# Kernel optimization log

Measured on AMD Instinct MI355X. Metric: run time of the kernel, lower is better.

## Reference

```python
import jax, jax.numpy as jnp
import numpy as np

EPS = 1e-20
TEMP = 0.07
PATCH = 64
STEP = 32  # patch_size * overlap(0.5)


def zero_softmax(x, eps=1e-5):
    # ZeroSoftmax: ((exp(x)-1)^2) / (sum + eps), maps x==0 -> exactly 0 weight
    e = jnp.square(jnp.exp(x) - 1.0)
    return e / (jnp.sum(e, axis=-1, keepdims=True) + eps)


def _scaling_mask(H, W, p, step):
    # constant overlap-count mask from CRW.compute_scaling_mask (static shapes)
    sm = np.zeros((H, W), np.float32)
    for i in range(0, H - step, step):
        for j in range(0, W - step, step):
            sm[i:i + p, j:j + p] += 1.0
    return jnp.asarray(sm)


def _window_sums(m, p, step):
    # m: (B,T,SP,H,W) -> sliding-window sums (B,T,SP,nH,nW) via integral image
    ii = jnp.cumsum(jnp.cumsum(m, axis=-2), axis=-1)
    ii = jnp.pad(ii, ((0, 0), (0, 0), (0, 0), (1, 0), (1, 0)))
    H = m.shape[-2]
    nH = (H - p) // step + 1
    lo = jnp.arange(nH) * step
    hi = lo + p
    r_hi = ii[..., hi, :]   # (B,T,SP,nH,W+1)
    r_lo = ii[..., lo, :]
    return r_hi[..., hi] - r_hi[..., lo] - r_lo[..., hi] + r_lo[..., lo]


def setup_inputs() -> dict:
    key = jax.random.key(0)
    k1, k2, k3 = jax.random.split(key, 3)
    B, T, H, W = 2, 4, 256, 256
    nH = (H - PATCH) // STEP + 1  # 7
    N = nH * nH                   # 49 patches
    Cenc, D, SP = 512, 128, 64
    feats = jax.random.normal(k1, (B, N, Cenc, T), jnp.float32)
    W_head = jax.random.normal(k2, (Cenc, D), jnp.float32) / np.sqrt(Cenc)
    sp_mask = jax.random.randint(k3, (B, T, H, W), 0, SP, jnp.int32)
    return {"feats": feats, "W_head": W_head, "sp_mask": sp_mask, "max_sp_num": SP}


def reference(feats, W_head, sp_mask, max_sp_num):
    B, N, Cenc, T = feats.shape
    H, W = sp_mask.shape[-2:]
    SP = max_sp_num

    # --- pixels_to_nodes tail: projection head + L2 normalize over channel dim ---
    q = jnp.einsum('bnct,cd->bndt', feats, W_head)            # (B,N,128,T)
    nrm = jnp.maximum(jnp.linalg.norm(q, axis=2, keepdims=True), 1e-12)
    q = q / nrm
    q = jnp.transpose(q, (0, 2, 3, 1))                        # (B,128,T,N)

    # --- patches_to_sp_embeddings: windowed superpixel pooling ---
    oh = (sp_mask[:, :, None, :, :] ==
          jnp.arange(SP, dtype=sp_mask.dtype)[None, None, :, None, None]
          ).astype(jnp.float32)                               # (B,T,SP,H,W)
    sm = _scaling_mask(H, W, PATCH, STEP)                     # (H,W)
    ws = _window_sums(oh / sm, PATCH, STEP)                   # (B,T,SP,nH,nW)
    denom = jnp.sum(oh, axis=(-1, -2)) + EPS                  # (B,T,SP)
    wts = jnp.transpose(ws, (0, 1, 3, 4, 2)) / denom[:, :, None, None, :]
    wts = wts.reshape(B, T, N, SP)                            # (B,T,N,SP)
    q_sp = jnp.einsum('bdtn,btns->bdts', q, wts)              # (B,128,T,SP)

    # --- affinity + zero_softmax stochastic matrices ---
    As = jnp.einsum('bdtn,bdtm->btnm', q_sp[:, :, :-1], q_sp[:, :, 1:])  # (B,T-1,SP,SP)
    A12 = zero_softmax(As / TEMP)
    A21 = zero_softmax(jnp.swapaxes(As, -1, -2) / TEMP)

    # --- palindrome random walks + cross-entropy to cycle-consistency targets ---
    tgt = jnp.tile(jnp.arange(SP), B)
    loss = jnp.float32(0.0)
    AAs = []
    for i in range(1, T - 1):
        mats = [A12[:, k] for k in range(i + 1)] + [A21[:, k] for k in range(i, -1, -1)]
        aa = mats[0]
        for m in mats[1:]:
            aa = aa @ m
        AAs.append(aa)
        logits = jnp.log(aa + EPS).reshape(B * SP, SP)
        logp = jax.nn.log_softmax(logits, axis=-1)
        loss = loss + jnp.mean(-logp[jnp.arange(B * SP), tgt])
    return loss, jnp.stack(AAs)
```

## Files before the change

kernel.cpp:

```cpp
#include <hip/hip_runtime.h>
#include <hip/hip_bf16.h>

constexpr int NWIN = 49;
constexpr int QLD  = 52;

constexpr int OFF_WS   = 0;
constexpr int OFF_Q    = 26624;
constexpr int OFF_QSP  = 79872;
constexpr int OFF_A12  = 145408;
constexpr int OFF_A12T = 169984;
constexpr int OFF_A21  = 194560;
constexpr int OFF_A21T = 219136;
constexpr int OFF_R1T  = 251904;
constexpr int OFF_L    = 260096;
constexpr int OFF_BAR  = 276480;

__global__ void __launch_bounds__(256, 1)
k_front(const int* __restrict__ mask, const float* __restrict__ feats,
        const float* __restrict__ Wh, float* __restrict__ ws, float* __restrict__ q) {
    if (blockIdx.x < 392) {
        int win = blockIdx.x % NWIN;
        int bt  = blockIdx.x / NWIN;
        int wy = win / 7, wx = win % 7;
        __shared__ float loc[64];
        if (threadIdx.x < 64) loc[threadIdx.x] = 0.f;
        __syncthreads();
        const int* base = mask + bt * 65536 + (wy * 32) * 256 + wx * 32;
        #pragma unroll
        for (int it = 0; it < 16; ++it) {
            int idx = it * 256 + (int)threadIdx.x;
            int r = idx >> 6, c = idx & 63;
            int s = base[r * 256 + c];
            int y = wy * 32 + r, x = wx * 32 + c;
            float w = 1.f;
            if (y >= 32 && y < 224) w *= 0.5f;
            if (x >= 32 && x < 224) w *= 0.5f;
            atomicAdd(&loc[s], w);
        }
        __syncthreads();
        if (threadIdx.x < 64) {
            ws[(bt * 64 + (int)threadIdx.x) * QLD + win] = loc[threadIdx.x];
        } else if (win == 0) {
            int s = threadIdx.x & 63;
            int col = 49 + (int)(threadIdx.x >> 6) - 1;
            ws[(bt * 64 + s) * QLD + col] = 0.f;
        }
    } else {
        int bid = blockIdx.x - 392;
        int n = bid % NWIN, b = bid / NWIN;
        __shared__ float4 f4[512];
        __shared__ float4 psum4[512];
        __shared__ float4 red4[2];
        const float4* fp4 = (const float4*)(feats + (size_t)(b * NWIN + n) * 2048);
        for (int i = threadIdx.x; i < 512; i += 256) f4[i] = fp4[i];
        __syncthreads();

        int dl = threadIdx.x & 63, ch = threadIdx.x >> 6;
        float a0 = 0.f, a1 = 0.f, a2 = 0.f, a3 = 0.f;
        float b0 = 0.f, b1 = 0.f, b2 = 0.f, b3 = 0.f;
        const float* wpa = Wh + dl;
        const float* wpb = Wh + dl + 64;
        int c0 = ch * 128;
        #pragma unroll 8
        for (int c = c0; c < c0 + 128; ++c) {
            float w0 = wpa[c * 128];
            float w1 = wpb[c * 128];
            float4 fv = f4[c];
            a0 += fv.x * w0; a1 += fv.y * w0; a2 += fv.z * w0; a3 += fv.w * w0;
            b0 += fv.x * w1; b1 += fv.y * w1; b2 += fv.z * w1; b3 += fv.w * w1;
        }
        psum4[ch * 128 + dl]      = make_float4(a0, a1, a2, a3);
        psum4[ch * 128 + dl + 64] = make_float4(b0, b1, b2, b3);
        __syncthreads();

        float4 A;
        if (threadIdx.x < 128) {
            float4 p0 = psum4[threadIdx.x],       p1 = psum4[128 + threadIdx.x];
            float4 p2 = psum4[256 + threadIdx.x], p3 = psum4[384 + threadIdx.x];
            A = make_float4((p0.x + p1.x) + (p2.x + p3.x),
                            (p0.y + p1.y) + (p2.y + p3.y),
                            (p0.z + p1.z) + (p2.z + p3.z),
                            (p0.w + p1.w) + (p2.w + p3.w));
            float sx = A.x * A.x, sy = A.y * A.y, sz = A.z * A.z, sw = A.w * A.w;
            for (int off = 32; off; off >>= 1) {
                sx += __shfl_down(sx, off); sy += __shfl_down(sy, off);
                sz += __shfl_down(sz, off); sw += __shfl_down(sw, off);
            }
            if ((threadIdx.x & 63) == 0) red4[threadIdx.x >> 6] = make_float4(sx, sy, sz, sw);
        }
        __syncthreads();
        if (threadIdx.x < 128) {
            float4 r0 = red4[0], r1 = red4[1];
            float ix = 1.f / fmaxf(sqrtf(r0.x + r1.x), 1e-12f);
            float iy = 1.f / fmaxf(sqrtf(r0.y + r1.y), 1e-12f);
            float iz = 1.f / fmaxf(sqrtf(r0.z + r1.z), 1e-12f);
            float iw = 1.f / fmaxf(sqrtf(r0.w + r1.w), 1e-12f);
            float* qb = q + (size_t)(b * 128 + (int)threadIdx.x) * 4 * QLD + n;
            qb[0 * QLD] = A.x * ix;
            qb[1 * QLD] = A.y * iy;
            qb[2 * QLD] = A.z * iz;
            qb[3 * QLD] = A.w * iw;
        }
    }
}

__global__ void k_qsp(const float* __restrict__ q, const float* __restrict__ wsg,
                      float* __restrict__ qsp, float* __restrict__ out,
                      int* __restrict__ bar) {
    if (blockIdx.x == 0 && threadIdx.x < 4) {
        bar[threadIdx.x] = 0;
        if (threadIdx.x == 0) out[0] = 0.f;
    }
    int gid = blockIdx.x * 256 + threadIdx.x;
    int d = gid & 127;
    int s = (gid >> 7) & 63;
    int t = (gid >> 13) & 3;
    int b = gid >> 15;
    const float4* qrow = (const float4*)(q + (size_t)((b * 128 + d) * 4 + t) * QLD);
    const float4* wrow = (const float4*)(wsg + (size_t)((b * 4 + t) * 64 + s) * QLD);
    float acc = 0.f, den = 0.f;
    #pragma unroll
    for (int i = 0; i < 13; ++i) {
        float4 w = wrow[i];
        float4 qv = qrow[i];
        den += w.x + w.y + w.z + w.w;
        acc += qv.x * w.x + qv.y * w.y + qv.z * w.z + qv.w * w.w;
    }
    int w = (s * 32 + ((d >> 2) ^ (s & 31))) * 4 + (d & 3);
    qsp[(size_t)(b * 4 + t) * 8192 + w] = acc / (den + 1e-20f);
}


__device__ __forceinline__ void dump_mat(float* M, const float4* v) {
    #pragma unroll
    for (int it = 0; it < 4; ++it) {
        int idx = it * 256 + (int)threadIdx.x;
        int r = idx >> 4, c4 = (idx & 15) << 2;
        *(float4*)&M[r * 64 + (c4 ^ ((r & 15) << 2))] = v[it];
    }
}

__device__ __forceinline__ void stage1(float* M, const float* __restrict__ G) {
    const float4* g = (const float4*)G;
    float4 v[4];
    #pragma unroll
    for (int it = 0; it < 4; ++it) v[it] = g[it * 256 + (int)threadIdx.x];
    dump_mat(M, v);
}

__device__ __forceinline__ void stage2(float* Ma, float* Mb,
                                       const float* __restrict__ Ga,
                                       const float* __restrict__ Gb) {
    const float4* ga = (const float4*)Ga;
    const float4* gb = (const float4*)Gb;
    float4 va[4], vb[4];
    #pragma unroll
    for (int it = 0; it < 4; ++it) {
        int idx = it * 256 + (int)threadIdx.x;
        va[it] = ga[idx];
        vb[it] = gb[idx];
    }
    dump_mat(Ma, va);
    dump_mat(Mb, vb);
}

__device__ __forceinline__ void mm256_sw(float* acc, const float* Ra, const float* Rb) {
    int tid = threadIdx.x;
    int nl = tid >> 4, ml = tid & 15;
    int sxa = nl << 2, sxb = ml << 2;
    #pragma unroll
    for (int i = 0; i < 16; ++i) acc[i] = 0.f;
    #pragma unroll 4
    for (int k0 = 0; k0 < 64; k0 += 4) {
        float4 av[4], bv[4];
        #pragma unroll
        for (int i = 0; i < 4; ++i)
            av[i] = *(const float4*)&Ra[(nl + 16 * i) * 64 + (k0 ^ sxa)];
        #pragma unroll
        for (int j = 0; j < 4; ++j)
            bv[j] = *(const float4*)&Rb[(ml + 16 * j) * 64 + (k0 ^ sxb)];
        #pragma unroll
        for (int i = 0; i < 4; ++i)
            #pragma unroll
            for (int j = 0; j < 4; ++j)
                acc[i * 4 + j] += av[i].x * bv[j].x + av[i].y * bv[j].y
                                + av[i].z * bv[j].z + av[i].w * bv[j].w;
    }
}

__device__ __forceinline__ void wr256_sw(float* M, const float* acc) {
    int nl = threadIdx.x >> 4, ml = threadIdx.x & 15;
    #pragma unroll
    for (int i = 0; i < 4; ++i)
        #pragma unroll
        for (int j = 0; j < 4; ++j) {
            int r = nl + 16 * i, k = ml + 16 * j;
            M[r * 64 + (((k & ~3) ^ ((r & 15) << 2)) | (k & 3))] = acc[i * 4 + j];
        }
}

__device__ __forceinline__ void store_mat(float* __restrict__ G, const float* acc) {
    int nl = threadIdx.x >> 4, ml = threadIdx.x & 15;
    #pragma unroll
    for (int i = 0; i < 4; ++i)
        #pragma unroll
        for (int j = 0; j < 4; ++j)
            G[(nl + 16 * i) * 64 + ml + 16 * j] = acc[i * 4 + j];
}

__device__ __forceinline__ void store_loss(const float* acc, float* __restrict__ aa,
                                           float* __restrict__ out, float* red) {
    int tid = threadIdx.x;
    int nl = tid >> 4, ml = tid & 15;
    #pragma unroll
    for (int i = 0; i < 4; ++i)
        #pragma unroll
        for (int j = 0; j < 4; ++j)
            aa[(nl + 16 * i) * 64 + (ml + 16 * j)] = acc[i * 4 + j];
    int l = tid & 63;
    float part = 0.f;
    #pragma unroll
    for (int i = 0; i < 4; ++i) {
        float rsum = acc[i * 4 + 0] + acc[i * 4 + 1] + acc[i * 4 + 2] + acc[i * 4 + 3];
        rsum += __shfl_down(rsum, 8, 16);
        rsum += __shfl_down(rsum, 4, 16);
        rsum += __shfl_down(rsum, 2, 16);
        rsum += __shfl_down(rsum, 1, 16);
        float dv = __shfl(acc[5 * i], (l & 48) | nl, 64);
        if ((l & 15) == 0) part += logf(rsum + 6.4e-19f) - logf(dv + 1e-20f);
    }
    for (int off = 32; off; off >>= 1) part += __shfl_down(part, off);
    if (l == 0) red[tid >> 6] = part;
    __syncthreads();
    if (tid == 0) atomicAdd(out, (red[0] + red[1] + red[2] + red[3]) * (1.f / 128.f));
}

__device__ __forceinline__ void gbar(int* cnt, int target) {
    __threadfence();
    __syncthreads();
    if (threadIdx.x == 0) {
        __hip_atomic_fetch_add(cnt, 1, __ATOMIC_ACQ_REL, __HIP_MEMORY_SCOPE_AGENT);
        while (__hip_atomic_load(cnt, __ATOMIC_ACQUIRE, __HIP_MEMORY_SCOPE_AGENT) < target)
            __builtin_amdgcn_s_sleep(2);
    }
    __syncthreads();
    __threadfence();
}

__global__ void __launch_bounds__(256, 1)
k_tail(const float* __restrict__ qsp,
       float* __restrict__ a12, float* __restrict__ a12T,
       float* __restrict__ a21, float* __restrict__ a21T,
       float* __restrict__ wsR1T, float* __restrict__ wsL,
       float* __restrict__ out, int* __restrict__ bar) {
    __shared__ float SM[16384];
    float* M0 = SM;
    float* M1 = SM + 4096;
    float* M2 = SM + 8192;
    float* M3 = SM + 12288;
    const int tid = threadIdx.x;
    const int blk = blockIdx.x;

    {
        int t = blk % 3, b = blk / 3;
        float4* qaT4 = (float4*)SM;
        float4* qbT4 = (float4*)SM + 2048;
        {
            const float4* gA = (const float4*)(qsp + (size_t)(b * 4 + t) * 8192);
            const float4* gB = (const float4*)(qsp + (size_t)(b * 4 + t + 1) * 8192);
            #pragma unroll
            for (int it = 0; it < 8; ++it) {
                int idx = it * 256 + tid;
                qaT4[idx] = gA[idx];
                qbT4[idx] = gB[idx];
            }
        }
        __syncthreads();

        const int nl = tid >> 4, ml = tid & 15;
        float acc[16];
        #pragma unroll
        for (int i = 0; i < 16; ++i) acc[i] = 0.f;
        #pragma unroll 8
        for (int k4 = 0; k4 < 32; ++k4) {
            float4 av[4], bv[4];
            #pragma unroll
            for (int i = 0; i < 4; ++i) { int n = nl + 16 * i; av[i] = qaT4[n * 32 + (k4 ^ (n & 31))]; }
            #pragma unroll
            for (int j = 0; j < 4; ++j) { int m = ml + 16 * j; bv[j] = qbT4[m * 32 + (k4 ^ (m & 31))]; }
            #pragma unroll
            for (int i = 0; i < 4; ++i)
                #pragma unroll
                for (int j = 0; j < 4; ++j)
                    acc[i * 4 + j] += av[i].x * bv[j].x + av[i].y * bv[j].y
                                    + av[i].z * bv[j].z + av[i].w * bv[j].w;
        }
        __syncthreads();

        float* eb = (float*)qaT4;
        float* rs = (float*)qbT4;
        float* cs = rs + 64;
        #pragma unroll
        for (int i = 0; i < 4; ++i)
            #pragma unroll
            for (int j = 0; j < 4; ++j) {
                int n = nl + 16 * i, m = ml + 16 * j;
                float x = acc[i * 4 + j] * (1.f / 0.07f);
                float e = expf(x) - 1.f;
                eb[n * 65 + m] = e * e;
            }
        __syncthreads();
        if (tid < 128) {
            int r = tid & 63; bool isrow = tid < 64;
            float a = 0.f;
            #pragma unroll
            for (int k = 0; k < 64; ++k) a += isrow ? eb[r * 65 + k] : eb[k * 65 + r];
            (isrow ? rs : cs)[r] = a + 1e-5f;
        }
        __syncthreads();
        float* p12  = a12  + (b * 3 + t) * 4096;
        float* p12T = a12T + (b * 3 + t) * 4096;
        float* p21  = a21  + (b * 3 + t) * 4096;
        float* p21T = a21T + (b * 3 + t) * 4096;
        #pragma unroll
        for (int i = 0; i < 4; ++i)
            #pragma unroll
            for (int j = 0; j < 4; ++j) {
                int n = nl + 16 * i, m = ml + 16 * j;
                float v   = eb[n * 65 + m];
                float v12 = v / rs[n];
                float v21 = v / cs[m];
                if (t == 0) {
                    p12 [n * 64 + m] = v12;
                    p21T[n * 64 + m] = v21;
                } else {
                    p12T[m * 64 + n] = v12;
                    p21 [m * 64 + n] = v21;
                }
            }
    }
    gbar(bar + 0, 6);
    if (blk >= 4) return;

    int b = blk >> 1, odd = blk & 1;
    if (!odd) {
        stage2(M0, M1, a12 + (b * 3 + 0) * 4096, a12T + (b * 3 + 1) * 4096);
        __syncthreads();
        float acc[16];
        mm256_sw(acc, M0, M1);
        wr256_sw(M2, acc);
        stage1(M3, a12T + (b * 3 + 2) * 4096);
        __syncthreads();
        float acc2[16];
        mm256_sw(acc2, M2, M3);
        store_mat(wsL + b * 4096, acc2);
    } else {
        stage2(M0, M1, a21T + (b * 3 + 0) * 4096, a21 + (b * 3 + 1) * 4096);
        __syncthreads();
        float acc[16];
        mm256_sw(acc, M0, M1);
        store_mat(wsR1T + b * 4096, acc);
        wr256_sw(M2, acc);
        stage1(M3, a21 + (b * 3 + 2) * 4096);
        __syncthreads();
        float acc2[16];
        mm256_sw(acc2, M2, M3);
        wr256_sw(M1, acc2);
    }
    gbar(bar + 1, 4);

    if (!odd) {
        stage1(M3, wsR1T + b * 4096);
        __syncthreads();
        float acc[16];
        mm256_sw(acc, M2, M3);
        store_loss(acc, out + 1 + b * 4096, out, M0);
    } else {
        stage1(M0, wsL + b * 4096);
        __syncthreads();
        float acc[16];
        mm256_sw(acc, M0, M1);
        store_loss(acc, out + 1 + (2 + b) * 4096, out, M2);
    }
}

extern "C" void kernel_launch(void* const* d_in, const int* in_sizes, int n_in,
                              void* d_out, int out_size, void* d_ws, size_t ws_size,
                              hipStream_t stream) {
    const float* feats = (const float*)d_in[0];
    const float* Wh    = (const float*)d_in[1];
    const int*   mask  = (const int*)d_in[2];
    float* out = (float*)d_out;
    float* ws  = (float*)d_ws;

    float* ws_sums = ws + OFF_WS;
    float* q       = ws + OFF_Q;
    float* qsp     = ws + OFF_QSP;
    float* a12     = ws + OFF_A12;
    float* a12T    = ws + OFF_A12T;
    float* a21     = ws + OFF_A21;
    float* a21T    = ws + OFF_A21T;
    float* wsR1T   = ws + OFF_R1T;
    float* wsL     = ws + OFF_L;
    int*   bar     = (int*)(ws + OFF_BAR);

    k_front<<<392 + 2 * NWIN, 256, 0, stream>>>(mask, feats, Wh, ws_sums, q);
    k_qsp<<<256, 256, 0, stream>>>(q, ws_sums, qsp, out, bar);
    k_tail<<<6, 256, 0, stream>>>(qsp, a12, a12T, a21, a21T,
                                  wsR1T, wsL, out, bar);
}
```

Measured before the change: 107.3 us.

## Fuse superpixel pooling kernel into tail kernel with an extra grid barrier

Removes the separate k_qsp launch and computes q_sp inside k_tail, now launched with 16 blocks. Each block stages a (b,t) slice of q and half of the window weights in LDS with an XOR swizzle and computes a 4x4 register tile per thread. Blocks then sync through a new global atomic barrier before the affinity stage. Barrier and output resets move into k_front. This removes one kernel launch and its gap, but adds a spin barrier and runs the pooling on only 16 blocks instead of 256.

```diff
diff --git a/kernel.cpp b/kernel.cpp
--- a/kernel.cpp
+++ b/kernel.cpp
@@ -17,8 +17,13 @@
 
 __global__ void __launch_bounds__(256, 1)
 k_front(const int* __restrict__ mask, const float* __restrict__ feats,
-        const float* __restrict__ Wh, float* __restrict__ ws, float* __restrict__ q) {
+        const float* __restrict__ Wh, float* __restrict__ ws, float* __restrict__ q,
+        float* __restrict__ out, int* __restrict__ bar) {
     if (blockIdx.x < 392) {
+        if (blockIdx.x == 0) {
+            if (threadIdx.x < 4) bar[threadIdx.x] = 0;
+            if (threadIdx.x == 4) out[0] = 0.f;
+        }
         int win = blockIdx.x % NWIN;
         int bt  = blockIdx.x / NWIN;
         int wy = win / 7, wx = win % 7;
@@ -104,32 +109,6 @@
     }
 }
 
-__global__ void k_qsp(const float* __restrict__ q, const float* __restrict__ wsg,
-                      float* __restrict__ qsp, float* __restrict__ out,
-                      int* __restrict__ bar) {
-    if (blockIdx.x == 0 && threadIdx.x < 4) {
-        bar[threadIdx.x] = 0;
-        if (threadIdx.x == 0) out[0] = 0.f;
-    }
-    int gid = blockIdx.x * 256 + threadIdx.x;
-    int d = gid & 127;
-    int s = (gid >> 7) & 63;
-    int t = (gid >> 13) & 3;
-    int b = gid >> 15;
-    const float4* qrow = (const float4*)(q + (size_t)((b * 128 + d) * 4 + t) * QLD);
-    const float4* wrow = (const float4*)(wsg + (size_t)((b * 4 + t) * 64 + s) * QLD);
-    float acc = 0.f, den = 0.f;
-    #pragma unroll
-    for (int i = 0; i < 13; ++i) {
-        float4 w = wrow[i];
-        float4 qv = qrow[i];
-        den += w.x + w.y + w.z + w.w;
-        acc += qv.x * w.x + qv.y * w.y + qv.z * w.z + qv.w * w.w;
-    }
-    int w = (s * 32 + ((d >> 2) ^ (s & 31))) * 4 + (d & 3);
-    qsp[(size_t)(b * 4 + t) * 8192 + w] = acc / (den + 1e-20f);
-}
-
 
 __device__ __forceinline__ void dump_mat(float* M, const float4* v) {
     #pragma unroll
@@ -248,7 +227,8 @@
 }
 
 __global__ void __launch_bounds__(256, 1)
-k_tail(const float* __restrict__ qsp,
+k_tail(const float* __restrict__ q, const float* __restrict__ wsg,
+       float* __restrict__ qsp,
        float* __restrict__ a12, float* __restrict__ a12T,
        float* __restrict__ a21, float* __restrict__ a21T,
        float* __restrict__ wsR1T, float* __restrict__ wsL,
@@ -260,6 +240,82 @@
     float* M3 = SM + 12288;
     const int tid = threadIdx.x;
     const int blk = blockIdx.x;
+
+    {
+        int bt = blk >> 1, hb = blk & 1;
+        float4* qL4 = (float4*)SM;
+        float4* wL4 = (float4*)SM + 1672;
+        const float4* qg = (const float4*)q + (size_t)((bt >> 2) * 512 + (bt & 3)) * 13;
+        const float4* wg = (const float4*)wsg + (size_t)(bt * 64 + hb * 32) * 13;
+        #pragma unroll
+        for (int it = 0; it < 7; ++it) {
+            int idx = it * 256 + tid;
+            if (idx < 1664) {
+                int d = idx / 13, k4 = idx - d * 13;
+                qL4[(d * 13 + k4) ^ ((d >> 2) & 7)] = qg[(size_t)d * 52 + k4];
+            }
+        }
+        #pragma unroll
+        for (int it = 0; it < 2; ++it) {
+            int idx = it * 256 + tid;
+            if (idx < 416) {
+                int sl = idx / 13, k4 = idx - sl * 13;
+                wL4[(sl * 13 + k4) ^ ((sl >> 2) & 7)] = wg[(size_t)sl * 13 + k4];
+            }
+        }
+        __syncthreads();
+
+        int dg = tid >> 3;
+        int sq = tid & 7;
+        float acc[4][4];
+        float den[4] = {0.f, 0.f, 0.f, 0.f};
+        #pragma unroll
+        for (int i = 0; i < 4; ++i)
+            #pragma unroll
+            for (int j = 0; j < 4; ++j) acc[i][j] = 0.f;
+        #pragma unroll
+        for (int k4 = 0; k4 < 13; ++k4) {
+            float4 av[4], bv[4];
+            #pragma unroll
+            for (int i = 0; i < 4; ++i)
+                av[i] = qL4[((dg * 4 + i) * 13 + k4) ^ (dg & 7)];
+            #pragma unroll
+            for (int j = 0; j < 4; ++j)
+                bv[j] = wL4[((sq * 4 + j) * 13 + k4) ^ (sq & 7)];
+            #pragma unroll
+            for (int j = 0; j < 4; ++j)
+                den[j] += bv[j].x + bv[j].y + bv[j].z + bv[j].w;
+            #pragma unroll
+            for (int i = 0; i < 4; ++i)
+                #pragma unroll
+                for (int j = 0; j < 4; ++j)
+                    acc[i][j] += av[i].x * bv[j].x + av[i].y * bv[j].y
+                               + av[i].z * bv[j].z + av[i].w * bv[j].w;
+        }
+        float4* qo = (float4*)qsp + (size_t)bt * 2048;
+        #pragma unroll
+        for (int j = 0; j < 4; ++j) {
+            int s = hb * 32 + sq * 4 + j;
+            float dn = den[j] + 1e-20f;
+            float4 o = make_float4(acc[0][j] / dn, acc[1][j] / dn,
+                                   acc[2][j] / dn, acc[3][j] / dn);
+            qo[s * 32 + (dg ^ (s & 31))] = o;
+        }
+    }
+    __threadfence();
+    __syncthreads();
+    if (blk >= 6) {
+        if (tid == 0)
+            __hip_atomic_fetch_add(bar + 0, 1, __ATOMIC_ACQ_REL, __HIP_MEMORY_SCOPE_AGENT);
+        return;
+    }
+    if (tid == 0) {
+        __hip_atomic_fetch_add(bar + 0, 1, __ATOMIC_ACQ_REL, __HIP_MEMORY_SCOPE_AGENT);
+        while (__hip_atomic_load(bar + 0, __ATOMIC_ACQUIRE, __HIP_MEMORY_SCOPE_AGENT) < 16)
+            __builtin_amdgcn_s_sleep(2);
+    }
+    __syncthreads();
+    __threadfence();
 
     {
         int t = blk % 3, b = blk / 3;
@@ -339,7 +395,7 @@
                 }
             }
     }
-    gbar(bar + 0, 6);
+    gbar(bar + 1, 6);
     if (blk >= 4) return;
 
     int b = blk >> 1, odd = blk & 1;
@@ -367,7 +423,7 @@
         mm256_sw(acc2, M2, M3);
         wr256_sw(M1, acc2);
     }
-    gbar(bar + 1, 4);
+    gbar(bar + 2, 4);
 
     if (!odd) {
         stage1(M3, wsR1T + b * 4096);
@@ -404,8 +460,7 @@
     float* wsL     = ws + OFF_L;
     int*   bar     = (int*)(ws + OFF_BAR);
 
-    k_front<<<392 + 2 * NWIN, 256, 0, stream>>>(mask, feats, Wh, ws_sums, q);
-    k_qsp<<<256, 256, 0, stream>>>(q, ws_sums, qsp, out, bar);
-    k_tail<<<6, 256, 0, stream>>>(qsp, a12, a12T, a21, a21T,
-                                  wsR1T, wsL, out, bar);
-}
+    k_front<<<392 + 2 * NWIN, 256, 0, stream>>>(mask, feats, Wh, ws_sums, q, out, bar);
+    k_tail<<<16, 256, 0, stream>>>(q, ws_sums, qsp, a12, a12T, a21, a21T,
+                                   wsR1T, wsL, out, bar);
+}
```

After: 113.8 us. +6.0%, slower.

## Keep locally produced stochastic matrices in LDS and remap tail blocks

Applied to the files above, without the earlier changes.

The tail kernel's chain products now run on blocks t=0 and t=1 of each batch instead of blocks 0-3. Each of those blocks writes its own freshly computed A12 (t=0) or A21 (t=1) directly into swizzled shared memory, so it no longer makes a global round trip through the workspace after the grid barrier. The global barrier now issues its fences from a single thread instead of all threads. The cost removed is global stores and reloads plus fence overhead on a tiny, latency-bound 6-block kernel. In exchange the swizzled LDS write is a scalar scatter that may bank-conflict, and the single-thread fence relies on __syncthreads for memory ordering.

```diff
diff --git a/kernel.cpp b/kernel.cpp
--- a/kernel.cpp
+++ b/kernel.cpp
@@ -7,7 +7,6 @@
 constexpr int OFF_WS   = 0;
 constexpr int OFF_Q    = 26624;
 constexpr int OFF_QSP  = 79872;
-constexpr int OFF_A12  = 145408;
 constexpr int OFF_A12T = 169984;
 constexpr int OFF_A21  = 194560;
 constexpr int OFF_A21T = 219136;
@@ -148,22 +147,6 @@
     dump_mat(M, v);
 }
 
-__device__ __forceinline__ void stage2(float* Ma, float* Mb,
-                                       const float* __restrict__ Ga,
-                                       const float* __restrict__ Gb) {
-    const float4* ga = (const float4*)Ga;
-    const float4* gb = (const float4*)Gb;
-    float4 va[4], vb[4];
-    #pragma unroll
-    for (int it = 0; it < 4; ++it) {
-        int idx = it * 256 + (int)threadIdx.x;
-        va[it] = ga[idx];
-        vb[it] = gb[idx];
-    }
-    dump_mat(Ma, va);
-    dump_mat(Mb, vb);
-}
-
 __device__ __forceinline__ void mm256_sw(float* acc, const float* Ra, const float* Rb) {
     int tid = threadIdx.x;
     int nl = tid >> 4, ml = tid & 15;
@@ -236,21 +219,20 @@
 }
 
 __device__ __forceinline__ void gbar(int* cnt, int target) {
-    __threadfence();
     __syncthreads();
     if (threadIdx.x == 0) {
+        __threadfence();
         __hip_atomic_fetch_add(cnt, 1, __ATOMIC_ACQ_REL, __HIP_MEMORY_SCOPE_AGENT);
         while (__hip_atomic_load(cnt, __ATOMIC_ACQUIRE, __HIP_MEMORY_SCOPE_AGENT) < target)
             __builtin_amdgcn_s_sleep(2);
+        __threadfence();
     }
     __syncthreads();
-    __threadfence();
 }
 
 __global__ void __launch_bounds__(256, 1)
 k_tail(const float* __restrict__ qsp,
-       float* __restrict__ a12, float* __restrict__ a12T,
-       float* __restrict__ a21, float* __restrict__ a21T,
+       float* __restrict__ a12T, float* __restrict__ a21, float* __restrict__ a21T,
        float* __restrict__ wsR1T, float* __restrict__ wsL,
        float* __restrict__ out, int* __restrict__ bar) {
     __shared__ float SM[16384];
@@ -260,9 +242,9 @@
     float* M3 = SM + 12288;
     const int tid = threadIdx.x;
     const int blk = blockIdx.x;
+    const int t = blk % 3, b = blk / 3;
 
     {
-        int t = blk % 3, b = blk / 3;
         float4* qaT4 = (float4*)SM;
         float4* qbT4 = (float4*)SM + 2048;
         {
@@ -318,7 +300,6 @@
             (isrow ? rs : cs)[r] = a + 1e-5f;
         }
         __syncthreads();
-        float* p12  = a12  + (b * 3 + t) * 4096;
         float* p12T = a12T + (b * 3 + t) * 4096;
         float* p21  = a21  + (b * 3 + t) * 4096;
         float* p21T = a21T + (b * 3 + t) * 4096;
@@ -331,8 +312,11 @@
                 float v12 = v / rs[n];
                 float v21 = v / cs[m];
                 if (t == 0) {
-                    p12 [n * 64 + m] = v12;
+                    M3[n * 64 + (((m & ~3) ^ ((n & 15) << 2)) | (m & 3))] = v12;
                     p21T[n * 64 + m] = v21;
+                } else if (t == 1) {
+                    p12T[m * 64 + n] = v12;
+                    M3[m * 64 + (((n & ~3) ^ ((m & 15) << 2)) | (n & 3))] = v21;
                 } else {
                     p12T[m * 64 + n] = v12;
                     p21 [m * 64 + n] = v21;
@@ -340,47 +324,47 @@
             }
     }
     gbar(bar + 0, 6);
-    if (blk >= 4) return;
-
-    int b = blk >> 1, odd = blk & 1;
+    if (t == 2) return;
+    const bool odd = (t == 1);
+
     if (!odd) {
-        stage2(M0, M1, a12 + (b * 3 + 0) * 4096, a12T + (b * 3 + 1) * 4096);
+        stage1(M0, a12T + (b * 3 + 1) * 4096);
+        __syncthreads();
+        float accP[16];
+        mm256_sw(accP, M3, M0);
+        wr256_sw(M1, accP);
+        stage1(M2, a12T + (b * 3 + 2) * 4096);
+        __syncthreads();
+        float accL[16];
+        mm256_sw(accL, M1, M2);
+        store_mat(wsL + b * 4096, accL);
+    } else {
+        stage1(M0, a21T + (b * 3 + 0) * 4096);
+        __syncthreads();
+        float accR[16];
+        mm256_sw(accR, M0, M3);
+        store_mat(wsR1T + b * 4096, accR);
+        wr256_sw(M1, accR);
+        stage1(M2, a21 + (b * 3 + 2) * 4096);
+        __syncthreads();
+        float accRT[16];
+        mm256_sw(accRT, M1, M2);
+        wr256_sw(M0, accRT);
+    }
+    gbar(bar + 1, 4);
+
+    if (!odd) {
+        stage1(M2, wsR1T + b * 4096);
         __syncthreads();
         float acc[16];
-        mm256_sw(acc, M0, M1);
-        wr256_sw(M2, acc);
-        stage1(M3, a12T + (b * 3 + 2) * 4096);
-        __syncthreads();
-        float acc2[16];
-        mm256_sw(acc2, M2, M3);
-        store_mat(wsL + b * 4096, acc2);
-    } else {
-        stage2(M0, M1, a21T + (b * 3 + 0) * 4096, a21 + (b * 3 + 1) * 4096);
-        __syncthreads();
-        float acc[16];
-        mm256_sw(acc, M0, M1);
-        store_mat(wsR1T + b * 4096, acc);
-        wr256_sw(M2, acc);
-        stage1(M3, a21 + (b * 3 + 2) * 4096);
-        __syncthreads();
-        float acc2[16];
-        mm256_sw(acc2, M2, M3);
-        wr256_sw(M1, acc2);
-    }
-    gbar(bar + 1, 4);
-
-    if (!odd) {
-        stage1(M3, wsR1T + b * 4096);
-        __syncthreads();
-        float acc[16];
-        mm256_sw(acc, M2, M3);
+        mm256_sw(acc, M1, M2);
         store_loss(acc, out + 1 + b * 4096, out, M0);
     } else {
-        stage1(M0, wsL + b * 4096);
+        stage1(M2, wsL + b * 4096);
         __syncthreads();
         float acc[16];
-        mm256_sw(acc, M0, M1);
-        store_loss(acc, out + 1 + (2 + b) * 4096, out, M2);
+        mm256_sw(acc, M2, M0);
+        store_loss(acc, out + 1 + (2 + b) * 4096, out, M1);
     }
 }
 
@@ -396,7 +380,6 @@
     float* ws_sums = ws + OFF_WS;
     float* q       = ws + OFF_Q;
     float* qsp     = ws + OFF_QSP;
-    float* a12     = ws + OFF_A12;
     float* a12T    = ws + OFF_A12T;
     float* a21     = ws + OFF_A21;
     float* a21T    = ws + OFF_A21T;
@@ -406,6 +389,6 @@
 
     k_front<<<392 + 2 * NWIN, 256, 0, stream>>>(mask, feats, Wh, ws_sums, q);
     k_qsp<<<256, 256, 0, stream>>>(q, ws_sums, qsp, out, bar);
-    k_tail<<<6, 256, 0, stream>>>(qsp, a12, a12T, a21, a21T,
+    k_tail<<<6, 256, 0, stream>>>(qsp, a12T, a21, a21T,
                                   wsR1T, wsL, out, bar);
 }
```

New measurement: 105.8 us. No clear change (-1.4%).
